# Optimization experiments

Hardware: AMD Instinct MI355X
Metric: run time of the kernel (lower is better)

## Reference

```python
import jax, jax.numpy as jnp
import numpy as np

SCALING = 2.5
OFFSET = 0.0
TIME_LENGTH = 10.0
DT = 0.1
CUTOFF = TIME_LENGTH  # cutoff=None -> time_length
TIME_STEPS = int(TIME_LENGTH // DT) + 1  # == 100 (float floor: 10.0//0.1 == 99.0)
CENTERS = np.array([-1.75, -1.25, -0.75, -0.25, 0.25, 0.75, 1.25, 1.75], dtype=np.float32)


def setup_inputs() -> dict:
    key = jax.random.key(0)
    k1, = jax.random.split(key, 1)
    trace = jax.random.normal(k1, (1024, 128), dtype=jnp.float32)
    center = jnp.asarray(CENTERS)
    return {"trace": trace, "center": center, "dummy1": 0, "dummy2": 0}


def reference(trace, center, dummy1, dummy2):
    B = trace.shape[0]
    # times: [B, F*C] latency per (feature, center) pair
    times = SCALING * jnp.abs(trace[..., None] - center).reshape(B, -1)
    times = jnp.where((times < 0) | (times > CUTOFF), TIME_LENGTH + DT, times)
    times = times + OFFSET
    bins = (times / DT + 1).astype(jnp.int32)  # trunc == floor for positive values
    mask = bins < TIME_STEPS
    N = times.shape[1]
    bi = jnp.broadcast_to(jnp.arange(B)[:, None], (B, N))
    ni = jnp.broadcast_to(jnp.arange(N)[None, :], (B, N))
    bins_c = jnp.clip(bins, 0, TIME_STEPS - 1)
    vals = mask.astype(jnp.int32)
    # masked scatter-add into pre-zeroed dense spike tensor (COO to_dense sums dups)
    spikes = jnp.zeros((TIME_STEPS, B, N), dtype=jnp.int32).at[bins_c, bi, ni].add(vals)
    return spikes
```

## Files before the change

### kernel.cpp

```cpp
#include <hip/hip_runtime.h>


#define BB 1024
#define FF 128
#define TT 100
#define PLANE_GROUPS ((BB * 1024) / 4)
#define TOTAL_GROUPS (TT * PLANE_GROUPS)
#define SWEEP_BLOCKS 512
#define SWEEP_STRIDE (SWEEP_BLOCKS * 256)
#define SWEEP_ITERS (TOTAL_GROUPS / SWEEP_STRIDE)

typedef int iv4 __attribute__((ext_vector_type(4)));

__global__ __launch_bounds__(256) void arnold_bins_kernel(
        const float* __restrict__ trace,
        const float* __restrict__ center,
        uchar4* __restrict__ bins) {
    const int b   = blockIdx.x;
    const int tid = threadIdx.x;
    const int n0  = tid << 2;
    const int f   = n0 >> 3;
    const int c0  = n0 & 7;

    const float x = trace[b * FF + f];

    unsigned char v[4];
#pragma unroll
    for (int i = 0; i < 4; ++i) {
        float tms = 2.5f * fabsf(x - center[c0 + i]);
        unsigned bb = (tms > 10.0f) ? 255u : (unsigned)(tms / 0.1f + 1.0f);
        v[i] = (unsigned char)bb;
    }
    bins[(b << 8) + tid] = make_uchar4(v[0], v[1], v[2], v[3]);
}

__global__ __launch_bounds__(256) void arnold_sweep_kernel(
        const uchar4* __restrict__ bins,
        iv4* __restrict__ out) {
    unsigned g = blockIdx.x * 256u + threadIdx.x;
#pragma unroll 4
    for (int k = 0; k < SWEEP_ITERS; ++k) {
        const unsigned t = g >> 18;
        const uchar4 c = bins[g & (PLANE_GROUPS - 1)];
        iv4 v;
        v.x = (c.x == t) ? 1 : 0;
        v.y = (c.y == t) ? 1 : 0;
        v.z = (c.z == t) ? 1 : 0;
        v.w = (c.w == t) ? 1 : 0;
        __builtin_nontemporal_store(v, out + g);
        g += SWEEP_STRIDE;
    }
}

extern "C" void kernel_launch(void* const* d_in, const int* in_sizes, int n_in,
                              void* d_out, int out_size, void* d_ws, size_t ws_size,
                              hipStream_t stream) {
    const float* trace  = (const float*)d_in[0];
    const float* center = (const float*)d_in[1];
    uchar4* bins = (uchar4*)d_ws;
    iv4* out = (iv4*)d_out;

    arnold_bins_kernel<<<BB, 256, 0, stream>>>(trace, center, bins);
    arnold_sweep_kernel<<<SWEEP_BLOCKS, 256, 0, stream>>>(bins, out);
}
```

Baseline: 411.5 us.

## Fuse bin computation into sweep kernel, keeping per-thread bins in registers

Merges the bin-computation kernel and the plane sweep into one kernel. Each thread computes bins for two batch rows (b and b+512) in registers, then loops over all 100 time steps writing one-hot int4 vectors with nontemporal stores. This removes the workspace round-trip, the repeated bin loads per time step and one kernel launch. In exchange each thread now writes two strided planes per iteration instead of one contiguous grid-stride stream.

```diff
diff --git a/kernel.cpp b/kernel.cpp
--- a/kernel.cpp
+++ b/kernel.cpp
@@ -1,54 +1,54 @@
 #include <hip/hip_runtime.h>
 
 
-#define BB 1024
 #define FF 128
 #define TT 100
-#define PLANE_GROUPS ((BB * 1024) / 4)
-#define TOTAL_GROUPS (TT * PLANE_GROUPS)
+#define PLANE_GROUPS ((1024 * 1024) / 4)
+#define HALF_PLANE (PLANE_GROUPS / 2)
 #define SWEEP_BLOCKS 512
-#define SWEEP_STRIDE (SWEEP_BLOCKS * 256)
-#define SWEEP_ITERS (TOTAL_GROUPS / SWEEP_STRIDE)
 
 typedef int iv4 __attribute__((ext_vector_type(4)));
 
-__global__ __launch_bounds__(256) void arnold_bins_kernel(
+__global__ __launch_bounds__(256) void arnold_sweep_fused(
         const float* __restrict__ trace,
         const float* __restrict__ center,
-        uchar4* __restrict__ bins) {
-    const int b   = blockIdx.x;
+        iv4* __restrict__ out) {
+    const int b0  = blockIdx.x;
     const int tid = threadIdx.x;
-    const int n0  = tid << 2;
-    const int f   = n0 >> 3;
-    const int c0  = n0 & 7;
+    const int f   = tid >> 1;
+    const int c0  = (tid & 1) << 2;
 
-    const float x = trace[b * FF + f];
+    float cc[4];
+#pragma unroll
+    for (int j = 0; j < 4; ++j) cc[j] = center[c0 + j];
 
-    unsigned char v[4];
+    const float x0 = trace[b0 * FF + f];
+    const float x1 = trace[(b0 + 512) * FF + f];
+
+    unsigned bin0[4], bin1[4];
 #pragma unroll
-    for (int i = 0; i < 4; ++i) {
-        float tms = 2.5f * fabsf(x - center[c0 + i]);
-        unsigned bb = (tms > 10.0f) ? 255u : (unsigned)(tms / 0.1f + 1.0f);
-        v[i] = (unsigned char)bb;
+    for (int j = 0; j < 4; ++j) {
+        float t0 = 2.5f * fabsf(x0 - cc[j]);
+        bin0[j] = (t0 > 10.0f) ? 255u : (unsigned)(t0 / 0.1f + 1.0f);
+        float t1 = 2.5f * fabsf(x1 - cc[j]);
+        bin1[j] = (t1 > 10.0f) ? 255u : (unsigned)(t1 / 0.1f + 1.0f);
     }
-    bins[(b << 8) + tid] = make_uchar4(v[0], v[1], v[2], v[3]);
-}
 
-__global__ __launch_bounds__(256) void arnold_sweep_kernel(
-        const uchar4* __restrict__ bins,
-        iv4* __restrict__ out) {
-    unsigned g = blockIdx.x * 256u + threadIdx.x;
+    iv4* p = out + (unsigned)(b0 * 256 + tid);
 #pragma unroll 4
-    for (int k = 0; k < SWEEP_ITERS; ++k) {
-        const unsigned t = g >> 18;
-        const uchar4 c = bins[g & (PLANE_GROUPS - 1)];
-        iv4 v;
-        v.x = (c.x == t) ? 1 : 0;
-        v.y = (c.y == t) ? 1 : 0;
-        v.z = (c.z == t) ? 1 : 0;
-        v.w = (c.w == t) ? 1 : 0;
-        __builtin_nontemporal_store(v, out + g);
-        g += SWEEP_STRIDE;
+    for (unsigned t = 0; t < TT; ++t) {
+        iv4 v0, v1;
+        v0.x = (bin0[0] == t) ? 1 : 0;
+        v0.y = (bin0[1] == t) ? 1 : 0;
+        v0.z = (bin0[2] == t) ? 1 : 0;
+        v0.w = (bin0[3] == t) ? 1 : 0;
+        v1.x = (bin1[0] == t) ? 1 : 0;
+        v1.y = (bin1[1] == t) ? 1 : 0;
+        v1.z = (bin1[2] == t) ? 1 : 0;
+        v1.w = (bin1[3] == t) ? 1 : 0;
+        __builtin_nontemporal_store(v0, p);
+        __builtin_nontemporal_store(v1, p + HALF_PLANE);
+        p += PLANE_GROUPS;
     }
 }
 
@@ -57,9 +57,8 @@
                               hipStream_t stream) {
     const float* trace  = (const float*)d_in[0];
     const float* center = (const float*)d_in[1];
-    uchar4* bins = (uchar4*)d_ws;
     iv4* out = (iv4*)d_out;
+    (void)d_ws; (void)ws_size;
 
-    arnold_bins_kernel<<<BB, 256, 0, stream>>>(trace, center, bins);
-    arnold_sweep_kernel<<<SWEEP_BLOCKS, 256, 0, stream>>>(bins, out);
+    arnold_sweep_fused<<<SWEEP_BLOCKS, 256, 0, stream>>>(trace, center, out);
 }
```

Result: no change. 407.9 us (-0.9%).
